# Optimization experiments

Hardware: AMD Instinct MI355X
Metric: run time of the kernel (lower is better)

The kernel has to match this reference:

```python
import jax, jax.numpy as jnp
import numpy as np
import math

DIM = 1024
HEADS = 16
HEAD_DIM = DIM // HEADS
B, T = 4, 2048


def setup_inputs() -> dict:
    key = jax.random.key(0)
    ks = jax.random.split(key, 11)
    s = 1.0 / math.sqrt(DIM)
    return {
        "Q": jax.random.normal(ks[0], (B, T, DIM), jnp.float32),
        "K": jax.random.normal(ks[1], (B, T, DIM), jnp.float32),
        "V": jax.random.normal(ks[2], (B, T, DIM), jnp.float32),
        "Wq": jax.random.uniform(ks[3], (DIM, DIM), jnp.float32, -s, s),
        "bq": jax.random.uniform(ks[4], (DIM,), jnp.float32, -s, s),
        "Wk": jax.random.uniform(ks[5], (DIM, DIM), jnp.float32, -s, s),
        "bk": jax.random.uniform(ks[6], (DIM,), jnp.float32, -s, s),
        "Wv": jax.random.uniform(ks[7], (DIM, DIM), jnp.float32, -s, s),
        "bv": jax.random.uniform(ks[8], (DIM,), jnp.float32, -s, s),
        "Wo": jax.random.uniform(ks[9], (DIM, DIM), jnp.float32, -s, s),
        "bo": jax.random.uniform(ks[10], (DIM,), jnp.float32, -s, s),
    }


def reference(Q, K, V, Wq, bq, Wk, bk, Wv, bv, Wo, bo):
    # Linear projections (torch Linear: x @ W.T + b)
    q = Q @ Wq.T + bq  # [B,T,D]
    k = K @ Wk.T + bk
    v = V @ Wv.T + bv
    # split heads -> [B,H,T,hd]
    def split(x):
        return x.reshape(B, T, HEADS, HEAD_DIM).transpose(0, 2, 1, 3)
    qh, kh, vh = split(q), split(k), split(v)
    qh = qh / math.sqrt(HEAD_DIM)
    scores = jnp.einsum("bhtd,bhsd->bhts", qh, kh)  # [B,H,T,T]
    A = jax.nn.softmax(scores, axis=-1)  # dropout p=0 -> identity
    Oh = jnp.einsum("bhts,bhsd->bhtd", A, vh)  # [B,H,T,hd]
    O = Oh.transpose(0, 2, 1, 3).reshape(B, T, DIM)
    O = O @ Wo.T + bo
    weight = A.mean(axis=1)  # [B,T,T] averaged over heads
    return O, weight
```

## Files before the change

### kernel.cpp

```cpp
#include <hip/hip_runtime.h>
#include <stdint.h>

typedef __attribute__((ext_vector_type(8))) short bf16x8;
typedef __attribute__((ext_vector_type(4))) float f32x4;
typedef __attribute__((ext_vector_type(4))) unsigned int u32x4;

static constexpr int B_ = 4, T_ = 2048, D_ = 1024, H_ = 16, HD_ = 64;
static constexpr int BT_ = B_ * T_;
static constexpr float LOG2E_OVER_8 = 0.18033688011112042f;

#define DEV static __device__ __forceinline__

#define RAW_BAR() do { \
    __builtin_amdgcn_sched_barrier(0); \
    __builtin_amdgcn_s_barrier(); \
    __builtin_amdgcn_sched_barrier(0); \
} while (0)

DEV unsigned short f2bf(float f) {
    union { float f; uint32_t u; } v; v.f = f;
    uint32_t u = v.u;
    uint32_t r = (u + 0x7fffu + ((u >> 16) & 1u)) >> 16;
    return (unsigned short)r;
}

DEV uint32_t cvt_pk_bf16(float lo, float hi) {
    uint32_t r;
    asm("v_cvt_pk_bf16_f32 %0, %1, %2" : "=v"(r) : "v"(lo), "v"(hi));
    return r;
}

DEV float fexp2(float x) {
    float r;
    asm("v_exp_f32 %0, %1" : "=v"(r) : "v"(x));
    return r;
}

DEV void gll16(const void* g, void* l) {
    __builtin_amdgcn_global_load_lds(
        (const __attribute__((address_space(1))) void*)g,
        (__attribute__((address_space(3))) void*)l, 16, 0, 0);
}

__global__ __launch_bounds__(256)
void cast_fused(const float* __restrict__ q, const float* __restrict__ k, const float* __restrict__ v,
                const float* __restrict__ wq, const float* __restrict__ wk,
                const float* __restrict__ wv, const float* __restrict__ wo,
                unsigned short* __restrict__ oq, unsigned short* __restrict__ ok,
                unsigned short* __restrict__ ov, unsigned short* __restrict__ owq,
                unsigned short* __restrict__ owk, unsigned short* __restrict__ owv,
                unsigned short* __restrict__ owo) {
    const int y = blockIdx.y;
    const float* s; unsigned short* d; int n4;
    switch (y) {
        case 0: s = q;  d = oq;  n4 = BT_ * D_ / 4; break;
        case 1: s = k;  d = ok;  n4 = BT_ * D_ / 4; break;
        case 2: s = v;  d = ov;  n4 = BT_ * D_ / 4; break;
        case 3: s = wq; d = owq; n4 = D_ * D_ / 4; break;
        case 4: s = wk; d = owk; n4 = D_ * D_ / 4; break;
        case 5: s = wv; d = owv; n4 = D_ * D_ / 4; break;
        default: s = wo; d = owo; n4 = D_ * D_ / 4; break;
    }
    for (int i = blockIdx.x * blockDim.x + threadIdx.x; i < n4; i += gridDim.x * blockDim.x) {
        float4 vv = reinterpret_cast<const float4*>(s)[i];
        ushort4 o;
        o.x = f2bf(vv.x); o.y = f2bf(vv.y); o.z = f2bf(vv.z); o.w = f2bf(vv.w);
        reinterpret_cast<ushort4*>(d)[i] = o;
    }
}

__global__ __launch_bounds__(256, 3)
void gemm_qkv(const unsigned short* __restrict__ Aq, const unsigned short* __restrict__ Ak,
              const unsigned short* __restrict__ Av,
              const unsigned short* __restrict__ Wqb, const unsigned short* __restrict__ Wkb,
              const unsigned short* __restrict__ Wvb,
              const float* __restrict__ bq, const float* __restrict__ bk,
              const float* __restrict__ bv,
              unsigned short* __restrict__ oq, unsigned short* __restrict__ ok,
              unsigned short* __restrict__ vT) {
    constexpr int K = 1024, N = 1024, BK = 64;
    __shared__ unsigned short sA[128 * BK];
    __shared__ unsigned short sB[128 * BK];
    const int flat = blockIdx.x + (blockIdx.y << 3) + (blockIdx.z << 9);
    const int nbz = (flat & 7) * 192 + (flat >> 3);
    const int z = nbz >> 9;
    const int rem = nbz & 511;
    const int bm = rem >> 3, bn = rem & 7;

    const unsigned short* A = z == 0 ? Aq : z == 1 ? Ak : Av;
    const unsigned short* W = z == 0 ? Wqb : z == 1 ? Wkb : Wvb;
    const float* bias        = z == 0 ? bq : z == 1 ? bk : bv;
    const float oscale       = z == 0 ? LOG2E_OVER_8 : 1.0f;

    const int tid = threadIdx.x;
    const int lane = tid & 63, w = tid >> 6;
    const int c = lane & 15, g = lane >> 4;
    const int wr = w >> 1, wc = w & 1;
    const int rowA0 = bm * 128, rowB0 = bn * 128;

    f32x4 acc[4][4] = {};

    for (int k0 = 0; k0 < K; k0 += BK) {
        __syncthreads();
#pragma unroll
        for (int i = 0; i < 4; ++i) {
            int chunk = tid + i * 256;
            int row = chunk >> 3, c16 = chunk & 7;
            int sc16 = c16 ^ (row & 7);
            gll16(A + (size_t)(rowA0 + row) * K + k0 + sc16 * 8, (char*)sA + chunk * 16);
            gll16(W + (size_t)(rowB0 + row) * K + k0 + sc16 * 8, (char*)sB + chunk * 16);
        }
        __syncthreads();
#pragma unroll
        for (int kk = 0; kk < 2; ++kk) {
            bf16x8 af[4], bfr[4];
#pragma unroll
            for (int mf = 0; mf < 4; ++mf) {
                int row = wr * 64 + mf * 16 + c;
                int off = (row * 128 + kk * 64 + g * 16) ^ ((row & 7) << 4);
                af[mf] = *reinterpret_cast<const bf16x8*>((const char*)sA + off);
            }
#pragma unroll
            for (int nf = 0; nf < 4; ++nf) {
                int row = wc * 64 + nf * 16 + c;
                int off = (row * 128 + kk * 64 + g * 16) ^ ((row & 7) << 4);
                bfr[nf] = *reinterpret_cast<const bf16x8*>((const char*)sB + off);
            }
#pragma unroll
            for (int mf = 0; mf < 4; ++mf)
#pragma unroll
                for (int nf = 0; nf < 4; ++nf)
                    acc[mf][nf] = __builtin_amdgcn_mfma_f32_16x16x32_bf16(af[mf], bfr[nf], acc[mf][nf], 0, 0, 0);
        }
    }

    if (z == 2) {
#pragma unroll
        for (int mf = 0; mf < 4; ++mf) {
            int rowbase = rowA0 + wr * 64 + mf * 16 + g * 4;
            int bb = rowbase >> 11;
            int trow = rowbase & 2047;
            int blk = trow >> 6, off = trow & 63;
            int slot = (off & 32) | ((off & 8) << 1) | ((off & 4) << 1) | ((off & 16) >> 2);
#pragma unroll
            for (int nf = 0; nf < 4; ++nf) {
                int col = rowB0 + wc * 64 + nf * 16 + c;
                float bvv = bias[col];
                int hh = col >> 6, d = col & 63;
                ushort4 o;
                o.x = f2bf(acc[mf][nf][0] + bvv);
                o.y = f2bf(acc[mf][nf][1] + bvv);
                o.z = f2bf(acc[mf][nf][2] + bvv);
                o.w = f2bf(acc[mf][nf][3] + bvv);
                size_t addr = (((size_t)(bb * H_ + hh)) * HD_ + d) * T_ + blk * 64 + slot;
                *reinterpret_cast<ushort4*>(&vT[addr]) = o;
            }
        }
    } else {
        unsigned short* out = z == 0 ? oq : ok;
#pragma unroll
        for (int mf = 0; mf < 4; ++mf)
#pragma unroll
            for (int nf = 0; nf < 4; ++nf) {
                int col = rowB0 + wc * 64 + nf * 16 + c;
                float bvv = bias[col];
#pragma unroll
                for (int j = 0; j < 4; ++j) {
                    int row = rowA0 + wr * 64 + mf * 16 + g * 4 + j;
                    float v = (acc[mf][nf][j] + bvv) * oscale;
                    out[(size_t)row * N + col] = f2bf(v);
                }
            }
    }
}

__global__ __launch_bounds__(256, 3)
void gemm_o(const unsigned short* __restrict__ A, const unsigned short* __restrict__ W,
            const float* __restrict__ bias, float* __restrict__ out) {
    constexpr int K = 1024, N = 1024, BK = 64;
    __shared__ unsigned short sA[128 * BK];
    __shared__ unsigned short sB[128 * BK];
    const int tid = threadIdx.x;
    const int lane = tid & 63, w = tid >> 6;
    const int c = lane & 15, g = lane >> 4;
    const int flat = blockIdx.x + (blockIdx.y << 3);
    const int nbz = (flat & 7) * 64 + (flat >> 3);
    const int bm = nbz >> 3, bn = nbz & 7;
    const int wr = w >> 1, wc = w & 1;
    const int rowA0 = bm * 128, rowB0 = bn * 128;

    f32x4 acc[4][4] = {};

    for (int k0 = 0; k0 < K; k0 += BK) {
        __syncthreads();
#pragma unroll
        for (int i = 0; i < 4; ++i) {
            int chunk = tid + i * 256;
            int row = chunk >> 3, c16 = chunk & 7;
            int sc16 = c16 ^ (row & 7);
            gll16(A + (size_t)(rowA0 + row) * K + k0 + sc16 * 8, (char*)sA + chunk * 16);
            gll16(W + (size_t)(rowB0 + row) * K + k0 + sc16 * 8, (char*)sB + chunk * 16);
        }
        __syncthreads();
#pragma unroll
        for (int kk = 0; kk < 2; ++kk) {
            bf16x8 af[4], bfr[4];
#pragma unroll
            for (int mf = 0; mf < 4; ++mf) {
                int row = wr * 64 + mf * 16 + c;
                int off = (row * 128 + kk * 64 + g * 16) ^ ((row & 7) << 4);
                af[mf] = *reinterpret_cast<const bf16x8*>((const char*)sA + off);
            }
#pragma unroll
            for (int nf = 0; nf < 4; ++nf) {
                int row = wc * 64 + nf * 16 + c;
                int off = (row * 128 + kk * 64 + g * 16) ^ ((row & 7) << 4);
                bfr[nf] = *reinterpret_cast<const bf16x8*>((const char*)sB + off);
            }
#pragma unroll
            for (int mf = 0; mf < 4; ++mf)
#pragma unroll
                for (int nf = 0; nf < 4; ++nf)
                    acc[mf][nf] = __builtin_amdgcn_mfma_f32_16x16x32_bf16(af[mf], bfr[nf], acc[mf][nf], 0, 0, 0);
        }
    }
#pragma unroll
    for (int mf = 0; mf < 4; ++mf)
#pragma unroll
        for (int nf = 0; nf < 4; ++nf) {
            int col = rowB0 + wc * 64 + nf * 16 + c;
            float bvv = bias[col];
#pragma unroll
            for (int j = 0; j < 4; ++j) {
                int row = rowA0 + wr * 64 + mf * 16 + g * 4 + j;
                out[(size_t)row * N + col] = acc[mf][nf][j] + bvv;
            }
        }
}

__global__ __launch_bounds__(256, 4)
void flash_kernel(const unsigned short* __restrict__ qbf,
                  const unsigned short* __restrict__ kbf,
                  const unsigned short* __restrict__ vT,
                  unsigned short* __restrict__ ohbf,
                  float* __restrict__ madjOut) {
    __shared__ unsigned short sK[2][64 * 64];
    __shared__ unsigned short sV[2][64 * 64];
    const int tid = threadIdx.x, lane = tid & 63, w = tid >> 6;
    const int c = lane & 15, g = lane >> 4;
    const int nb = (blockIdx.x & 7) * 128 + (blockIdx.x >> 3);
    const int t0 = (nb & 15) * 128, h = (nb >> 4) & 15, b = nb >> 8;

    bf16x8 qf[2][2];
#pragma unroll
    for (int u = 0; u < 2; ++u) {
        const size_t qbase = ((size_t)(b * T_) + t0 + w * 32 + u * 16 + c) * D_ + h * HD_;
        qf[u][0] = *reinterpret_cast<const bf16x8*>(qbf + qbase + g * 8);
        qf[u][1] = *reinterpret_cast<const bf16x8*>(qbf + qbase + 32 + g * 8);
    }

    const unsigned short one_bf = 0x3F80;
    const bf16x8 ones = { (short)one_bf, (short)one_bf, (short)one_bf, (short)one_bf,
                          (short)one_bf, (short)one_bf, (short)one_bf, (short)one_bf };

    f32x4 acc[2][4] = {};
    f32x4 acc_l[2] = {};

    const unsigned short* kRow = kbf + (size_t)b * T_ * D_ + h * HD_;
    const unsigned short* vRow = vT + ((size_t)(b * H_ + h)) * HD_ * T_;

    auto stage = [&](int buf, int s0) {
#pragma unroll
        for (int i = 0; i < 2; ++i) {
            int chunk = tid + i * 256;
            int row = chunk >> 3, c16 = chunk & 7;
            int sc16 = c16 ^ (row & 7);
            gll16(kRow + (size_t)(s0 + row) * D_ + sc16 * 8, (char*)sK[buf] + chunk * 16);
            gll16(vRow + (size_t)row * T_ + s0 + sc16 * 8, (char*)sV[buf] + chunk * 16);
        }
    };

    stage(0, 0);
    constexpr int NT = T_ / 64;

    for (int it = 0; it < NT; ++it) {
        const int cur = it & 1;
        if (it + 1 < NT) {
            stage(cur ^ 1, (it + 1) * 64);
            asm volatile("s_waitcnt vmcnt(4)" ::: "memory");
        } else {
            asm volatile("s_waitcnt vmcnt(0)" ::: "memory");
        }
        RAW_BAR();

        const char* sKc = (const char*)sK[cur];
        const char* sVc = (const char*)sV[cur];

        f32x4 sc[2][4] = {};
        __builtin_amdgcn_s_setprio(1);
#pragma unroll
        for (int kk = 0; kk < 2; ++kk)
#pragma unroll
            for (int nf = 0; nf < 4; ++nf) {
                int row = nf * 16 + c;
                int off = (row * 128 + kk * 64 + g * 16) ^ ((row & 7) << 4);
                bf16x8 kf = *reinterpret_cast<const bf16x8*>(sKc + off);
                sc[0][nf] = __builtin_amdgcn_mfma_f32_16x16x32_bf16(kf, qf[0][kk], sc[0][nf], 0, 0, 0);
                sc[1][nf] = __builtin_amdgcn_mfma_f32_16x16x32_bf16(kf, qf[1][kk], sc[1][nf], 0, 0, 0);
            }
        __builtin_amdgcn_s_setprio(0);

        u32x4 pkw[2][2];
#pragma unroll
        for (int u = 0; u < 2; ++u) {
#pragma unroll
            for (int nf = 0; nf < 4; ++nf)
#pragma unroll
                for (int j = 0; j < 4; ++j)
                    sc[u][nf][j] = fexp2(sc[u][nf][j]);
#pragma unroll
            for (int kk = 0; kk < 2; ++kk) {
                u32x4 pw;
                pw.x = cvt_pk_bf16(sc[u][2 * kk][0], sc[u][2 * kk][1]);
                pw.y = cvt_pk_bf16(sc[u][2 * kk][2], sc[u][2 * kk][3]);
                pw.z = cvt_pk_bf16(sc[u][2 * kk + 1][0], sc[u][2 * kk + 1][1]);
                pw.w = cvt_pk_bf16(sc[u][2 * kk + 1][2], sc[u][2 * kk + 1][3]);
                pkw[u][kk] = pw;
            }
        }

        __builtin_amdgcn_s_setprio(1);
#pragma unroll
        for (int kk = 0; kk < 2; ++kk) {
            bf16x8 pa0 = __builtin_bit_cast(bf16x8, pkw[0][kk]);
            bf16x8 pa1 = __builtin_bit_cast(bf16x8, pkw[1][kk]);
#pragma unroll
            for (int nf = 0; nf < 4; ++nf) {
                int row = nf * 16 + c;
                int voff = (row * 128 + kk * 64 + g * 16) ^ ((row & 7) << 4);
                bf16x8 vf = *reinterpret_cast<const bf16x8*>(sVc + voff);
                acc[0][nf] = __builtin_amdgcn_mfma_f32_16x16x32_bf16(pa0, vf, acc[0][nf], 0, 0, 0);
                acc[1][nf] = __builtin_amdgcn_mfma_f32_16x16x32_bf16(pa1, vf, acc[1][nf], 0, 0, 0);
            }
            acc_l[0] = __builtin_amdgcn_mfma_f32_16x16x32_bf16(pa0, ones, acc_l[0], 0, 0, 0);
            acc_l[1] = __builtin_amdgcn_mfma_f32_16x16x32_bf16(pa1, ones, acc_l[1], 0, 0, 0);
        }
        __builtin_amdgcn_s_setprio(0);
        RAW_BAR();
    }

#pragma unroll
    for (int u = 0; u < 2; ++u) {
#pragma unroll
        for (int j = 0; j < 4; ++j) {
            float inv = 1.f / acc_l[u][j];
            int trow = t0 + w * 32 + u * 16 + g * 4 + j;
#pragma unroll
            for (int nf = 0; nf < 4; ++nf)
                ohbf[((size_t)(b * T_) + trow) * D_ + h * HD_ + nf * 16 + c] = f2bf(acc[u][nf][j] * inv);
            if (c == 0)
                madjOut[((size_t)(b * H_ + h)) * T_ + trow] = 4.0f + __log2f(acc_l[u][j]);
        }
    }
}

__global__ __launch_bounds__(512, 4)
void weight_kernel(const unsigned short* __restrict__ qbf,
                   const unsigned short* __restrict__ kbf,
                   const float* __restrict__ madjIn,
                   float* __restrict__ wout) {
    __shared__ unsigned short sQ[2][128 * 64];
    __shared__ unsigned short sK2[2][128 * 64];
    __shared__ float sMadj[16][128];
    const int tid = threadIdx.x, lane = tid & 63, w = tid >> 6;
    const int c = lane & 15, g = lane >> 4;
    const int wr = w >> 2, wc = w & 3;
    const int nb = (blockIdx.x & 7) * 128 + (blockIdx.x >> 3);
    const int s0 = (nb & 15) * 128, t0 = ((nb >> 4) & 15) * 128, b = nb >> 8;

    float wacc[4][2][4] = {};

    auto stageW = [&](int buf, int h) {
#pragma unroll
        for (int i = 0; i < 2; ++i) {
            int chunk = tid + i * 512;
            int row = chunk >> 3, c16 = chunk & 7;
            int sc16 = c16 ^ (row & 7);
            gll16(qbf + ((size_t)(b * T_) + t0 + row) * D_ + h * HD_ + sc16 * 8,
                  (char*)sQ[buf] + chunk * 16);
        }
#pragma unroll
        for (int i = 0; i < 2; ++i) {
            int chunk = tid + i * 512;
            int row = chunk >> 3, c16 = chunk & 7;
            int sc16 = c16 ^ (row & 7);
            gll16(kbf + ((size_t)(b * T_) + s0 + row) * D_ + h * HD_ + sc16 * 8,
                  (char*)sK2[buf] + chunk * 16);
        }
    };

    {
        int hh = tid >> 5, tq = tid & 31;
        float4 mv = *reinterpret_cast<const float4*>(
            &madjIn[((size_t)(b * H_ + hh)) * T_ + t0 + tq * 4]);
        *reinterpret_cast<float4*>(&sMadj[hh][tq * 4]) = mv;
    }
    __syncthreads();

    stageW(0, 0);

    for (int h = 0; h < H_; ++h) {
        const int cur = h & 1;
        if (h + 1 < H_) {
            stageW(cur ^ 1, h + 1);
            asm volatile("s_waitcnt vmcnt(4)" ::: "memory");
        } else {
            asm volatile("s_waitcnt vmcnt(0)" ::: "memory");
        }
        RAW_BAR();

        const char* sQc = (const char*)sQ[cur];
        const char* sKc = (const char*)sK2[cur];

        f32x4 sc[4][2];
#pragma unroll
        for (int mf = 0; mf < 4; ++mf) {
            f32x4 mrow = *reinterpret_cast<const f32x4*>(&sMadj[h][wr * 64 + mf * 16 + g * 4]);
#pragma unroll
            for (int j = 0; j < 4; ++j) {
                sc[mf][0][j] = -mrow[j];
                sc[mf][1][j] = -mrow[j];
            }
        }

        __builtin_amdgcn_s_setprio(1);
#pragma unroll
        for (int kk = 0; kk < 2; ++kk) {
            bf16x8 af[4], bfr[2];
#pragma unroll
            for (int mf = 0; mf < 4; ++mf) {
                int row = wr * 64 + mf * 16 + c;
                int off = (row * 128 + kk * 64 + g * 16) ^ ((row & 7) << 4);
                af[mf] = *reinterpret_cast<const bf16x8*>(sQc + off);
            }
#pragma unroll
            for (int nf = 0; nf < 2; ++nf) {
                int row = wc * 32 + nf * 16 + c;
                int off = (row * 128 + kk * 64 + g * 16) ^ ((row & 7) << 4);
                bfr[nf] = *reinterpret_cast<const bf16x8*>(sKc + off);
            }
#pragma unroll
            for (int mf = 0; mf < 4; ++mf)
#pragma unroll
                for (int nf = 0; nf < 2; ++nf)
                    sc[mf][nf] = __builtin_amdgcn_mfma_f32_16x16x32_bf16(af[mf], bfr[nf], sc[mf][nf], 0, 0, 0);
        }
        __builtin_amdgcn_s_setprio(0);
#pragma unroll
        for (int mf = 0; mf < 4; ++mf)
#pragma unroll
            for (int nf = 0; nf < 2; ++nf)
#pragma unroll
                for (int j = 0; j < 4; ++j)
                    wacc[mf][nf][j] += fexp2(sc[mf][nf][j]);
        RAW_BAR();
    }
#pragma unroll
    for (int mf = 0; mf < 4; ++mf)
#pragma unroll
        for (int j = 0; j < 4; ++j) {
            int trow = t0 + wr * 64 + mf * 16 + g * 4 + j;
#pragma unroll
            for (int nf = 0; nf < 2; ++nf) {
                int col = s0 + wc * 32 + nf * 16 + c;
                wout[((size_t)b * T_ + trow) * (size_t)T_ + col] = wacc[mf][nf][j];
            }
        }
}

extern "C" void kernel_launch(void* const* d_in, const int* in_sizes, int n_in,
                              void* d_out, int out_size, void* d_ws, size_t ws_size,
                              hipStream_t stream) {
    const float* Q  = (const float*)d_in[0];
    const float* K  = (const float*)d_in[1];
    const float* V  = (const float*)d_in[2];
    const float* Wq = (const float*)d_in[3];
    const float* bq = (const float*)d_in[4];
    const float* Wk = (const float*)d_in[5];
    const float* bk = (const float*)d_in[6];
    const float* Wv = (const float*)d_in[7];
    const float* bv = (const float*)d_in[8];
    const float* Wo = (const float*)d_in[9];
    const float* bo = (const float*)d_in[10];

    char* ws = (char*)d_ws;
    const size_t MB = 1u << 20;
    unsigned short* Wqb = (unsigned short*)(ws);
    unsigned short* Wkb = Wqb + 1024 * 1024;
    unsigned short* Wvb = Wkb + 1024 * 1024;
    unsigned short* Wob = Wvb + 1024 * 1024;
    unsigned short* Qc  = (unsigned short*)(ws + 8 * MB);
    unsigned short* Kc  = (unsigned short*)(ws + 24 * MB);
    unsigned short* Vc  = (unsigned short*)(ws + 40 * MB);
    unsigned short* qb  = (unsigned short*)(ws + 56 * MB);
    unsigned short* kb  = (unsigned short*)(ws + 72 * MB);
    unsigned short* vT  = (unsigned short*)(ws + 88 * MB);
    unsigned short* ohb = Kc;
    float* mArr = (float*)(ws + 104 * MB);

    cast_fused<<<dim3(1024, 7), 256, 0, stream>>>(Q, K, V, Wq, Wk, Wv, Wo,
                                                  Qc, Kc, Vc, Wqb, Wkb, Wvb, Wob);

    gemm_qkv<<<dim3(8, 64, 3), 256, 0, stream>>>(Qc, Kc, Vc, Wqb, Wkb, Wvb,
                                                 bq, bk, bv, qb, kb, vT);

    flash_kernel<<<1024, 256, 0, stream>>>(qb, kb, vT, ohb, mArr);

    float* Oout = (float*)d_out;
    float* Wout = Oout + (size_t)BT_ * D_;
    gemm_o<<<dim3(8, 64), 256, 0, stream>>>(ohb, Wob, bo, Oout);
    weight_kernel<<<1024, 512, 0, stream>>>(qb, kb, mArr, Wout);
}
```

Measured before the change: 250.2 us.

## Fuse fp32-to-bf16 activation cast into QKV GEMM tile loads

Removes the separate cast of the Q, K, V activations to bf16 and instead has the QKV GEMM read fp32 activations directly. It converts them to packed bf16 in registers and stores them into swizzled shared memory. The cast kernel now only handles the four weight matrices. This avoids writing and re-reading three 16MB bf16 activation buffers. The cost is that the A-tile loads become synchronous register loads instead of async global-to-LDS loads. Each A element is also re-read and re-converted by all 8 N-tile blocks, which doubles A read bytes per block.

After: 253.0 us. Within noise of the previous version (+1.1%).

```diff
diff --git a/kernel.cpp b/kernel.cpp
--- a/kernel.cpp
+++ b/kernel.cpp
@@ -43,24 +43,19 @@
 }
 
 __global__ __launch_bounds__(256)
-void cast_fused(const float* __restrict__ q, const float* __restrict__ k, const float* __restrict__ v,
-                const float* __restrict__ wq, const float* __restrict__ wk,
+void cast_fused(const float* __restrict__ wq, const float* __restrict__ wk,
                 const float* __restrict__ wv, const float* __restrict__ wo,
-                unsigned short* __restrict__ oq, unsigned short* __restrict__ ok,
-                unsigned short* __restrict__ ov, unsigned short* __restrict__ owq,
-                unsigned short* __restrict__ owk, unsigned short* __restrict__ owv,
-                unsigned short* __restrict__ owo) {
+                unsigned short* __restrict__ owq, unsigned short* __restrict__ owk,
+                unsigned short* __restrict__ owv, unsigned short* __restrict__ owo) {
     const int y = blockIdx.y;
-    const float* s; unsigned short* d; int n4;
+    const float* s; unsigned short* d;
     switch (y) {
-        case 0: s = q;  d = oq;  n4 = BT_ * D_ / 4; break;
-        case 1: s = k;  d = ok;  n4 = BT_ * D_ / 4; break;
-        case 2: s = v;  d = ov;  n4 = BT_ * D_ / 4; break;
-        case 3: s = wq; d = owq; n4 = D_ * D_ / 4; break;
-        case 4: s = wk; d = owk; n4 = D_ * D_ / 4; break;
-        case 5: s = wv; d = owv; n4 = D_ * D_ / 4; break;
-        default: s = wo; d = owo; n4 = D_ * D_ / 4; break;
-    }
+        case 0: s = wq; d = owq; break;
+        case 1: s = wk; d = owk; break;
+        case 2: s = wv; d = owv; break;
+        default: s = wo; d = owo; break;
+    }
+    const int n4 = D_ * D_ / 4;
     for (int i = blockIdx.x * blockDim.x + threadIdx.x; i < n4; i += gridDim.x * blockDim.x) {
         float4 vv = reinterpret_cast<const float4*>(s)[i];
         ushort4 o;
@@ -70,8 +65,8 @@
 }
 
 __global__ __launch_bounds__(256, 3)
-void gemm_qkv(const unsigned short* __restrict__ Aq, const unsigned short* __restrict__ Ak,
-              const unsigned short* __restrict__ Av,
+void gemm_qkv(const float* __restrict__ Aq, const float* __restrict__ Ak,
+              const float* __restrict__ Av,
               const unsigned short* __restrict__ Wqb, const unsigned short* __restrict__ Wkb,
               const unsigned short* __restrict__ Wvb,
               const float* __restrict__ bq, const float* __restrict__ bk,
@@ -87,7 +82,7 @@
     const int rem = nbz & 511;
     const int bm = rem >> 3, bn = rem & 7;
 
-    const unsigned short* A = z == 0 ? Aq : z == 1 ? Ak : Av;
+    const float* A = z == 0 ? Aq : z == 1 ? Ak : Av;
     const unsigned short* W = z == 0 ? Wqb : z == 1 ? Wkb : Wvb;
     const float* bias        = z == 0 ? bq : z == 1 ? bk : bv;
     const float oscale       = z == 0 ? LOG2E_OVER_8 : 1.0f;
@@ -107,8 +102,22 @@
             int chunk = tid + i * 256;
             int row = chunk >> 3, c16 = chunk & 7;
             int sc16 = c16 ^ (row & 7);
-            gll16(A + (size_t)(rowA0 + row) * K + k0 + sc16 * 8, (char*)sA + chunk * 16);
             gll16(W + (size_t)(rowB0 + row) * K + k0 + sc16 * 8, (char*)sB + chunk * 16);
+        }
+#pragma unroll
+        for (int i = 0; i < 4; ++i) {
+            int chunk = tid + i * 256;
+            int row = chunk >> 3, c16 = chunk & 7;
+            int sc16 = c16 ^ (row & 7);
+            const float* src = A + (size_t)(rowA0 + row) * K + k0 + sc16 * 8;
+            float4 lo = *reinterpret_cast<const float4*>(src);
+            float4 hi = *reinterpret_cast<const float4*>(src + 4);
+            u32x4 pk;
+            pk.x = cvt_pk_bf16(lo.x, lo.y);
+            pk.y = cvt_pk_bf16(lo.z, lo.w);
+            pk.z = cvt_pk_bf16(hi.x, hi.y);
+            pk.w = cvt_pk_bf16(hi.z, hi.w);
+            *reinterpret_cast<u32x4*>((char*)sA + chunk * 16) = pk;
         }
         __syncthreads();
 #pragma unroll
@@ -499,19 +508,15 @@
     unsigned short* Wkb = Wqb + 1024 * 1024;
     unsigned short* Wvb = Wkb + 1024 * 1024;
     unsigned short* Wob = Wvb + 1024 * 1024;
-    unsigned short* Qc  = (unsigned short*)(ws + 8 * MB);
-    unsigned short* Kc  = (unsigned short*)(ws + 24 * MB);
-    unsigned short* Vc  = (unsigned short*)(ws + 40 * MB);
+    unsigned short* ohb = (unsigned short*)(ws + 24 * MB);
     unsigned short* qb  = (unsigned short*)(ws + 56 * MB);
     unsigned short* kb  = (unsigned short*)(ws + 72 * MB);
     unsigned short* vT  = (unsigned short*)(ws + 88 * MB);
-    unsigned short* ohb = Kc;
     float* mArr = (float*)(ws + 104 * MB);
 
-    cast_fused<<<dim3(1024, 7), 256, 0, stream>>>(Q, K, V, Wq, Wk, Wv, Wo,
-                                                  Qc, Kc, Vc, Wqb, Wkb, Wvb, Wob);
-
-    gemm_qkv<<<dim3(8, 64, 3), 256, 0, stream>>>(Qc, Kc, Vc, Wqb, Wkb, Wvb,
+    cast_fused<<<dim3(256, 4), 256, 0, stream>>>(Wq, Wk, Wv, Wo, Wqb, Wkb, Wvb, Wob);
+
+    gemm_qkv<<<dim3(8, 64, 3), 256, 0, stream>>>(Q, K, V, Wqb, Wkb, Wvb,
                                                  bq, bk, bv, qb, kb, vT);
 
     flash_kernel<<<1024, 256, 0, stream>>>(qb, kb, vT, ohb, mArr);
```
